# Performance work log

Measured on AMD Instinct MI355X. Metric: run time of the kernel, lower is better.

Reference implementation:

```python
import jax, jax.numpy as jnp
import numpy as np

D_MODEL = 512
N_HEADS = 8
D_HEAD = D_MODEL // N_HEADS
D_FF = 2048
LN_EPS = 1e-5


def _layer_norm(x, g, b):
    mu = jnp.mean(x, axis=-1, keepdims=True)
    var = jnp.var(x, axis=-1, keepdims=True)
    return (x - mu) * jax.lax.rsqrt(var + LN_EPS) * g + b


def setup_inputs() -> dict:
    key = jax.random.key(0)
    ks = jax.random.split(key, 16)
    s_d = 1.0 / np.sqrt(D_MODEL)
    s_f = 1.0 / np.sqrt(D_FF)
    x = jax.random.normal(ks[0], (32, 512, D_MODEL), dtype=jnp.float32)
    # per-head Q/K/V linears stacked over heads: [H, D, dh] weights, [H, dh] biases
    Wq = jax.random.uniform(ks[1], (N_HEADS, D_MODEL, D_HEAD), jnp.float32, -s_d, s_d)
    bq = jax.random.uniform(ks[2], (N_HEADS, D_HEAD), jnp.float32, -s_d, s_d)
    Wk = jax.random.uniform(ks[3], (N_HEADS, D_MODEL, D_HEAD), jnp.float32, -s_d, s_d)
    bk = jax.random.uniform(ks[4], (N_HEADS, D_HEAD), jnp.float32, -s_d, s_d)
    Wv = jax.random.uniform(ks[5], (N_HEADS, D_MODEL, D_HEAD), jnp.float32, -s_d, s_d)
    bv = jax.random.uniform(ks[6], (N_HEADS, D_HEAD), jnp.float32, -s_d, s_d)
    Wo = jax.random.uniform(ks[7], (D_MODEL, D_MODEL), jnp.float32, -s_d, s_d)
    bo = jax.random.uniform(ks[8], (D_MODEL,), jnp.float32, -s_d, s_d)
    ln1_g = jnp.ones((D_MODEL,), jnp.float32)
    ln1_b = jnp.zeros((D_MODEL,), jnp.float32)
    W1 = jax.random.uniform(ks[9], (D_MODEL, D_FF), jnp.float32, -s_d, s_d)
    b1 = jax.random.uniform(ks[10], (D_FF,), jnp.float32, -s_d, s_d)
    W2 = jax.random.uniform(ks[11], (D_FF, D_MODEL), jnp.float32, -s_f, s_f)
    b2 = jax.random.uniform(ks[12], (D_MODEL,), jnp.float32, -s_f, s_f)
    ln2_g = jnp.ones((D_MODEL,), jnp.float32)
    ln2_b = jnp.zeros((D_MODEL,), jnp.float32)
    return dict(x=x, Wq=Wq, bq=bq, Wk=Wk, bk=bk, Wv=Wv, bv=bv, Wo=Wo, bo=bo,
                ln1_g=ln1_g, ln1_b=ln1_b, W1=W1, b1=b1, W2=W2, b2=b2,
                ln2_g=ln2_g, ln2_b=ln2_b)


def reference(x, Wq, bq, Wk, bk, Wv, bv, Wo, bo, ln1_g, ln1_b, W1, b1, W2, b2, ln2_g, ln2_b):
    B, T, D = x.shape
    # batched-heads Q/K/V: [B, H, T, dh]
    q = jnp.einsum('btd,hde->bhte', x, Wq) + bq[None, :, None, :]
    k = jnp.einsum('btd,hde->bhte', x, Wk) + bk[None, :, None, :]
    v = jnp.einsum('btd,hde->bhte', x, Wv) + bv[None, :, None, :]
    scale = D_HEAD ** -0.5
    scores = jnp.einsum('bhte,bhse->bhts', q, k) * scale  # [B,H,T,T]
    causal = jnp.tril(jnp.ones((T, T), dtype=bool))
    scores = jnp.where(causal[None, None], scores, -jnp.inf)
    w = jax.nn.softmax(scores, axis=-1)
    o = jnp.einsum('bhts,bhse->bhte', w, v)              # [B,H,T,dh]
    o = jnp.transpose(o, (0, 2, 1, 3)).reshape(B, T, D)   # concat heads
    attn = o @ Wo + bo
    out1 = x + _layer_norm(attn, ln1_g, ln1_b)            # post-LN on sublayer output (as in source)
    ff = jax.nn.relu(out1 @ W1 + b1) @ W2 + b2
    return out1 + _layer_norm(ff, ln2_g, ln2_b)
```

## Files before the change

### kernel.cpp

```cpp
#include <hip/hip_runtime.h>
#include <hip/hip_bf16.h>


#define D_MODEL 512
#define N_HEADS 8
#define D_HEAD 64
#define D_FF 2048
#define NROWS 16384

typedef __bf16 bf16x8 __attribute__((ext_vector_type(8)));
typedef float f32x4 __attribute__((ext_vector_type(4)));

#define SWZ(x) ((x) ^ ((((x) >> 7) & 7) << 4))

static __device__ __forceinline__ ushort f2bf(float f) {
    union { float f; unsigned u; } v; v.f = f;
    unsigned r = v.u + 0x7fffu + ((v.u >> 16) & 1u);
    return (ushort)(r >> 16);
}
static __device__ __forceinline__ unsigned pack2(float lo, float hi) {
    return (unsigned)f2bf(lo) | ((unsigned)f2bf(hi) << 16);
}
static __device__ __forceinline__ void async16(const void* g, void* l) {
    __builtin_amdgcn_global_load_lds(
        (const __attribute__((address_space(1))) void*)g,
        (__attribute__((address_space(3))) void*)l, 16, 0, 0);
}

__global__ __launch_bounds__(256) void conv_bf_kernel(
    const float* __restrict__ src, ushort* __restrict__ dst, int n8)
{
    int i = blockIdx.x * 256 + threadIdx.x;
    if (i >= n8) return;
    const float4* s = (const float4*)src;
    float4 a = s[i * 2], b = s[i * 2 + 1];
    uint4 o;
    o.x = pack2(a.x, a.y); o.y = pack2(a.z, a.w);
    o.z = pack2(b.x, b.y); o.w = pack2(b.z, b.w);
    ((uint4*)dst)[i] = o;
}

static __device__ __forceinline__ void tile_transpose_body(
    const float* __restrict__ src, int srcldc, ushort* __restrict__ dst, int Rd,
    int r0, int c0)
{
    __shared__ float t[64][65];
    int tid = threadIdx.x;
    int lr = tid >> 4, lc4 = (tid & 15) * 4;
    #pragma unroll
    for (int i = 0; i < 4; ++i) {
        float4 v = *(const float4*)&src[(size_t)(r0 + lr + i * 16) * srcldc + c0 + lc4];
        t[lr + i * 16][lc4 + 0] = v.x;
        t[lr + i * 16][lc4 + 1] = v.y;
        t[lr + i * 16][lc4 + 2] = v.z;
        t[lr + i * 16][lc4 + 3] = v.w;
    }
    __syncthreads();
    int oc = tid >> 2, orr = (tid & 3) * 16;
    uint4 u0, u1;
    u0.x = pack2(t[orr + 0][oc],  t[orr + 1][oc]);
    u0.y = pack2(t[orr + 2][oc],  t[orr + 3][oc]);
    u0.z = pack2(t[orr + 4][oc],  t[orr + 5][oc]);
    u0.w = pack2(t[orr + 6][oc],  t[orr + 7][oc]);
    u1.x = pack2(t[orr + 8][oc],  t[orr + 9][oc]);
    u1.y = pack2(t[orr + 10][oc], t[orr + 11][oc]);
    u1.z = pack2(t[orr + 12][oc], t[orr + 13][oc]);
    u1.w = pack2(t[orr + 14][oc], t[orr + 15][oc]);
    ushort* d = dst + (size_t)(c0 + oc) * Rd + r0 + orr;
    *(uint4*)&d[0] = u0;
    *(uint4*)&d[8] = u1;
}

__global__ __launch_bounds__(256) void transpose_bf_kernel(
    const float* __restrict__ src, ushort* __restrict__ dst, int R, int C)
{
    tile_transpose_body(src, C, dst, R, blockIdx.y * 64, blockIdx.x * 64);
}

__global__ __launch_bounds__(256) void qkv_pack_kernel(
    const float* __restrict__ Wq, const float* __restrict__ Wk,
    const float* __restrict__ Wv, ushort* __restrict__ WpT)
{
    int z = blockIdx.z;
    int p = z >> 3, h = z & 7;
    const float* src = ((p == 0) ? Wq : (p == 1) ? Wk : Wv) + (size_t)h * D_MODEL * D_HEAD;
    ushort* dst = WpT + (size_t)(p * D_MODEL + h * D_HEAD) * D_MODEL;
    tile_transpose_body(src, D_HEAD, dst, D_MODEL, blockIdx.y * 64, 0);
}

__global__ __launch_bounds__(256) void pack_bias_kernel(
    const float* __restrict__ bq, const float* __restrict__ bk,
    const float* __restrict__ bv, float* __restrict__ bp)
{
    int idx = blockIdx.x * 256 + threadIdx.x;
    if (idx >= 3 * D_MODEL) return;
    int p = idx / D_MODEL;
    int h = (idx % D_MODEL) / D_HEAD;
    int e = idx % D_HEAD;
    const float* bb = (p == 0) ? bq : (p == 1) ? bk : bv;
    bp[idx] = bb[h * D_HEAD + e];
}

template<int OMODE, bool RELU>
__global__ __launch_bounds__(256) void gemm_bf16_kernel(
    const ushort* __restrict__ A, const ushort* __restrict__ BT,
    const float* __restrict__ bias, void* __restrict__ Cout,
    ushort* __restrict__ Qg, ushort* __restrict__ Kg, ushort* __restrict__ Vt,
    int M, int N, int K)
{
    __shared__ __align__(16) __bf16 As[128 * 64];
    __shared__ __align__(16) __bf16 Bs[128 * 64];

    const int tid = threadIdx.x;
    const int w = tid >> 6, l = tid & 63;
    const int wr = w >> 1, wc = w & 1;
    const int m0 = blockIdx.y * 128, n0 = blockIdx.x * 128;

    const ushort* Ag = A + (size_t)(m0 + w * 8 + l / 8) * K + (l % 8) * 8;
    const ushort* Bg = BT + (size_t)(n0 + w * 8 + l / 8) * K + (l % 8) * 8;
    __bf16* Asw = As + w * 512 + l * 8;
    __bf16* Bsw = Bs + w * 512 + l * 8;

    const int fr = l & 15, fq = l >> 4;
    const int a_base = (wr * 64 + fr) * 64 + fq * 8;
    const int b_base = (wc * 64 + fr) * 64 + fq * 8;

    f32x4 acc[4][4] = {};

    for (int k0 = 0; k0 < K; k0 += 64) {
        #pragma unroll
        for (int i = 0; i < 4; ++i) {
            async16(Ag + k0 + (size_t)i * 32 * K, Asw + i * 2048);
            async16(Bg + k0 + (size_t)i * 32 * K, Bsw + i * 2048);
        }
        __syncthreads();
        #pragma unroll
        for (int ks = 0; ks < 2; ++ks) {
            bf16x8 af[4], bfv[4];
            #pragma unroll
            for (int mi = 0; mi < 4; ++mi)
                af[mi] = *(const bf16x8*)&As[a_base + mi * 1024 + ks * 32];
            #pragma unroll
            for (int ni = 0; ni < 4; ++ni)
                bfv[ni] = *(const bf16x8*)&Bs[b_base + ni * 1024 + ks * 32];
            #pragma unroll
            for (int mi = 0; mi < 4; ++mi)
                #pragma unroll
                for (int ni = 0; ni < 4; ++ni)
                    acc[mi][ni] = __builtin_amdgcn_mfma_f32_16x16x32_bf16(
                        af[mi], bfv[ni], acc[mi][ni], 0, 0, 0);
        }
        __syncthreads();
    }

    #pragma unroll
    for (int ni = 0; ni < 4; ++ni) {
        int c = n0 + wc * 64 + ni * 16 + fr;
        float bv = bias ? bias[c] : 0.f;
        #pragma unroll
        for (int mi = 0; mi < 4; ++mi) {
            int r0 = m0 + wr * 64 + mi * 16 + fq * 4;
            float vv[4];
            #pragma unroll
            for (int reg = 0; reg < 4; ++reg) {
                float v = acc[mi][ni][reg] + bv;
                if (RELU) v = fmaxf(v, 0.f);
                vv[reg] = v;
            }
            if (OMODE == 0) {
                #pragma unroll
                for (int reg = 0; reg < 4; ++reg)
                    ((float*)Cout)[(size_t)(r0 + reg) * N + c] = vv[reg];
            } else if (OMODE == 1) {
                #pragma unroll
                for (int reg = 0; reg < 4; ++reg)
                    ((ushort*)Cout)[(size_t)(r0 + reg) * N + c] = f2bf(vv[reg]);
            } else {
                int p = n0 >> 9;
                int h = (c >> 6) & 7, e = c & 63;
                int b = r0 >> 9, t0 = r0 & 511;
                size_t bh = (size_t)(b * 8 + h);
                if (p == 2) {
                    uint2 pk;
                    pk.x = pack2(vv[0], vv[1]);
                    pk.y = pack2(vv[2], vv[3]);
                    *(uint2*)&Vt[bh * 32768 + (size_t)e * 512 + t0] = pk;
                } else {
                    ushort* dst = (p == 0 ? Qg : Kg) + bh * 32768 + (size_t)t0 * 64 + e;
                    #pragma unroll
                    for (int reg = 0; reg < 4; ++reg)
                        dst[reg * 64] = f2bf(vv[reg]);
                }
            }
        }
    }
}

__global__ __launch_bounds__(256) void attn_kernel(
    const ushort* __restrict__ Qg,
    const ushort* __restrict__ Kg,
    const ushort* __restrict__ Vt,
    ushort* __restrict__ O)
{
    __shared__ __align__(16) char QP[8192];
    __shared__ __align__(16) char KB[2][8192];
    __shared__ __align__(16) char VB[2][8192];

    const int bh = blockIdx.x, qb = blockIdx.y;
    const int tid = threadIdx.x;
    const int w = tid >> 6, l = tid & 63;

    const ushort* Qb = Qg + (size_t)bh * 32768;
    const ushort* Kb = Kg + (size_t)bh * 32768;
    const ushort* Vb = Vt + (size_t)bh * 32768;

    #pragma unroll
    for (int i = 0; i < 2; ++i) {
        int Xi = i * 4096 + tid * 16;
        int row = Xi >> 7;
        int sw = SWZ(Xi) & 127;
        async16((const char*)(Qb + (size_t)(qb * 64 + row) * 64) + sw, QP + Xi);
    }
    #define STAGEKV(kt, bb)                                                     \
        { _Pragma("unroll")                                                     \
          for (int i = 0; i < 2; ++i) {                                         \
              int Xi = i * 4096 + tid * 16;                                     \
              int row = Xi >> 7;                                                \
              int sw = SWZ(Xi) & 127;                                           \
              async16((const char*)(Kb + (size_t)((kt) * 64 + row) * 64) + sw,  \
                      KB[bb] + Xi);                                             \
              async16((const char*)(Vb + (size_t)row * 512 + (kt) * 64) + sw,   \
                      VB[bb] + Xi);                                             \
          } }
    STAGEKV(0, 0);
    __syncthreads();

    bf16x8 qf[2];
    {
        int qrow = w * 16 + (l & 15);
        #pragma unroll
        for (int ks = 0; ks < 2; ++ks) {
            int X = qrow * 128 + ks * 64 + (l >> 4) * 16;
            qf[ks] = *(const bf16x8*)(QP + SWZ(X));
        }
    }

    float mrow = -INFINITY, lrow = 0.f;
    f32x4 oacc[4] = {};
// ... 37 lines not shown
        float psum = 0.f;
        #pragma unroll
        for (int i = 0; i < 16; ++i) { sv[i] = __expf(sv[i] - mnew); psum += sv[i]; }
        psum += __shfl_xor(psum, 16);
        psum += __shfl_xor(psum, 32);
        lrow = lrow * corr + psum;

        #pragma unroll
        for (int mi = 0; mi < 4; ++mi) {
            uint2 pk;
            pk.x = pack2(sv[mi * 4 + 0], sv[mi * 4 + 1]);
            pk.y = pack2(sv[mi * 4 + 2], sv[mi * 4 + 3]);
            int X = qrow_t * 128 + (mi * 16 + (l >> 4) * 4) * 2;
            *(uint2*)(QP + SWZ(X)) = pk;
        }

        #pragma unroll
        for (int r = 0; r < 4; ++r) {
            float cr = __shfl(corr, (l & 48) | ((l >> 4) * 4 + r));
            #pragma unroll
            for (int n = 0; n < 4; ++n) oacc[n][r] *= cr;
        }

        #pragma unroll
        for (int ks = 0; ks < 2; ++ks) {
            int Xa = qrow_t * 128 + ks * 64 + (l >> 4) * 16;
            bf16x8 pa = *(const bf16x8*)(QP + SWZ(Xa));
            #pragma unroll
            for (int n = 0; n < 4; ++n) {
                int Xb = (n * 16 + (l & 15)) * 128 + ks * 64 + (l >> 4) * 16;
                bf16x8 vb = *(const bf16x8*)(VB[cur] + SWZ(Xb));
                oacc[n] = __builtin_amdgcn_mfma_f32_16x16x32_bf16(
                    pa, vb, oacc[n], 0, 0, 0);
            }
        }
        __syncthreads();
    }

    float linv = 1.0f / lrow;
    const int b_ = bh >> 3, h_ = bh & 7;
    #pragma unroll
    for (int r = 0; r < 4; ++r) {
        float li = __shfl(linv, (l & 48) | ((l >> 4) * 4 + r));
        int trow = qb * 64 + w * 16 + (l >> 4) * 4 + r;
        size_t obase = ((size_t)b_ * 512 + trow) * 512 + h_ * 64 + (l & 15);
        #pragma unroll
        for (int n = 0; n < 4; ++n)
            O[obase + n * 16] = f2bf(oacc[n][r] * li);
    }
}

template<bool WBF>
__global__ __launch_bounds__(256) void ln_res_kernel(
    const float* __restrict__ v, const float* __restrict__ res,
    const float* __restrict__ g, const float* __restrict__ bb,
    float* __restrict__ out, ushort* __restrict__ out_bf)
{
    int row  = blockIdx.x * 4 + (threadIdx.x >> 6);
    int lane = threadIdx.x & 63;
    const float4* vp = (const float4*)(v + (size_t)row * D_MODEL);
    float4 a = vp[lane];
    float4 c = vp[lane + 64];
    float sum = a.x + a.y + a.z + a.w + c.x + c.y + c.z + c.w;
    float sq  = a.x*a.x + a.y*a.y + a.z*a.z + a.w*a.w
              + c.x*c.x + c.y*c.y + c.z*c.z + c.w*c.w;
    #pragma unroll
    for (int o = 1; o < 64; o <<= 1) {
        sum += __shfl_xor(sum, o);
        sq  += __shfl_xor(sq, o);
    }
    float mu   = sum * (1.f / 512.f);
    float var  = sq * (1.f / 512.f) - mu * mu;
    float rstd = rsqrtf(var + 1e-5f);

    const float4* rp = (const float4*)(res + (size_t)row * D_MODEL);
    const float4* gp = (const float4*)g;
    const float4* bp = (const float4*)bb;
    float4 r0 = rp[lane], r1 = rp[lane + 64];
    float4 g0 = gp[lane], g1 = gp[lane + 64];
    float4 b0 = bp[lane], b1 = bp[lane + 64];
    float4 o0, o1;
    o0.x = r0.x + (a.x - mu) * rstd * g0.x + b0.x;
    o0.y = r0.y + (a.y - mu) * rstd * g0.y + b0.y;
    o0.z = r0.z + (a.z - mu) * rstd * g0.z + b0.z;
    o0.w = r0.w + (a.w - mu) * rstd * g0.w + b0.w;
    o1.x = r1.x + (c.x - mu) * rstd * g1.x + b1.x;
    o1.y = r1.y + (c.y - mu) * rstd * g1.y + b1.y;
    o1.z = r1.z + (c.z - mu) * rstd * g1.z + b1.z;
    o1.w = r1.w + (c.w - mu) * rstd * g1.w + b1.w;
    float4* op = (float4*)(out + (size_t)row * D_MODEL);
    op[lane] = o0;
    op[lane + 64] = o1;
    if (WBF) {
        uint2 p0, p1;
        p0.x = pack2(o0.x, o0.y); p0.y = pack2(o0.z, o0.w);
        p1.x = pack2(o1.x, o1.y); p1.y = pack2(o1.z, o1.w);
        *(uint2*)&out_bf[(size_t)row * D_MODEL + lane * 4] = p0;
        *(uint2*)&out_bf[(size_t)row * D_MODEL + 256 + lane * 4] = p1;
    }
}

extern "C" void kernel_launch(void* const* d_in, const int* in_sizes, int n_in,
                              void* d_out, int out_size, void* d_ws, size_t ws_size,
                              hipStream_t stream)
{
    const float* x     = (const float*)d_in[0];
    const float* Wq    = (const float*)d_in[1];
    const float* bq    = (const float*)d_in[2];
    const float* Wk    = (const float*)d_in[3];
    const float* bk    = (const float*)d_in[4];
    const float* Wv    = (const float*)d_in[5];
    const float* bv    = (const float*)d_in[6];
    const float* Wo    = (const float*)d_in[7];
    const float* bo    = (const float*)d_in[8];
    const float* ln1_g = (const float*)d_in[9];
    const float* ln1_b = (const float*)d_in[10];
    const float* W1    = (const float*)d_in[11];
    const float* b1    = (const float*)d_in[12];
    const float* W2    = (const float*)d_in[13];
    const float* b2    = (const float*)d_in[14];
    const float* ln2_g = (const float*)d_in[15];
    const float* ln2_b = (const float*)d_in[16];

    float* ws = (float*)d_ws;
    ushort* Qg      = (ushort*)(ws);
    ushort* Kg      = (ushort*)(ws + 4194304);
    ushort* Vt      = (ushort*)(ws + 8388608);
    ushort* O_bf    = (ushort*)(ws + 12582912);
    float*  attnb   = ws + 16777216;
    float*  out1    = ws + 25165824;
    ushort* out1_bf = (ushort*)(ws + 33554432);
    ushort* x_bf    = (ushort*)(ws + 37748736);
    ushort* WpT     = (ushort*)(ws + 41943040);
    ushort* WoT     = (ushort*)(ws + 42336256);
    ushort* W1T     = (ushort*)(ws + 42467328);
    ushort* W2T     = (ushort*)(ws + 42991616);
    float*  bp      = ws + 43515904;
    ushort* ff1_bf  = (ushort*)ws;
    float*  ff2     = attnb;

    conv_bf_kernel<<<dim3(4096), 256, 0, stream>>>(x, x_bf, NROWS * D_MODEL / 8);
    qkv_pack_kernel<<<dim3(1, 8, 24), 256, 0, stream>>>(Wq, Wk, Wv, WpT);
    transpose_bf_kernel<<<dim3(8, 8), 256, 0, stream>>>(Wo, WoT, 512, 512);
    transpose_bf_kernel<<<dim3(32, 8), 256, 0, stream>>>(W1, W1T, 512, 2048);
    transpose_bf_kernel<<<dim3(8, 32), 256, 0, stream>>>(W2, W2T, 2048, 512);
    pack_bias_kernel<<<dim3(6), 256, 0, stream>>>(bq, bk, bv, bp);

    gemm_bf16_kernel<2, false><<<dim3(12, 128), 256, 0, stream>>>(
        x_bf, WpT, bp, nullptr, Qg, Kg, Vt, NROWS, 1536, 512);

    attn_kernel<<<dim3(256, 8), 256, 0, stream>>>(Qg, Kg, Vt, O_bf);

    gemm_bf16_kernel<0, false><<<dim3(4, 128), 256, 0, stream>>>(
        O_bf, WoT, bo, attnb, nullptr, nullptr, nullptr, NROWS, 512, 512);

    ln_res_kernel<true><<<dim3(NROWS / 4), 256, 0, stream>>>(
        attnb, x, ln1_g, ln1_b, out1, out1_bf);

    gemm_bf16_kernel<1, true><<<dim3(16, 128), 256, 0, stream>>>(
        out1_bf, W1T, b1, ff1_bf, nullptr, nullptr, nullptr, NROWS, 2048, 512);

    gemm_bf16_kernel<0, false><<<dim3(4, 128), 256, 0, stream>>>(
        ff1_bf, W2T, b2, ff2, nullptr, nullptr, nullptr, NROWS, 512, 2048);

    ln_res_kernel<false><<<dim3(NROWS / 4), 256, 0, stream>>>(
        ff2, out1, ln2_g, ln2_b, (float*)d_out, nullptr);
}
```

Measured before the change: 264.0 us.

## Rewrite bf16 GEMM with double-buffered LDS, 32x32 MFMA, swizzle, larger tiles

The GEMM kernel now uses 256x128 tiles with 512 threads, 32x32x16 MFMA instructions, XOR-swizzled LDS layout, and a double-buffered async global-to-LDS pipeline that uses a single barrier per k-step. A flat grid with an XCD-aware block remap replaces the 2D grid. The aim is to overlap loads with MFMA compute, reduce LDS bank conflicts, and improve data reuse per block. In exchange it needs 96KB of dynamic shared memory per block, allowing only one block per CU, and the epilogue store pattern changes.

```diff
diff --git a/kernel.cpp b/kernel.cpp
--- a/kernel.cpp
+++ b/kernel.cpp
@@ -10,6 +10,7 @@
 
 typedef __bf16 bf16x8 __attribute__((ext_vector_type(8)));
 typedef float f32x4 __attribute__((ext_vector_type(4)));
+typedef float f32x16 __attribute__((ext_vector_type(16)));
 
 #define SWZ(x) ((x) ^ ((((x) >> 7) & 7) << 4))
 
@@ -102,98 +103,137 @@
 }
 
 template<int OMODE, bool RELU>
-__global__ __launch_bounds__(256) void gemm_bf16_kernel(
+__global__ __launch_bounds__(512, 1) void gemm_bf16_kernel(
     const ushort* __restrict__ A, const ushort* __restrict__ BT,
     const float* __restrict__ bias, void* __restrict__ Cout,
     ushort* __restrict__ Qg, ushort* __restrict__ Kg, ushort* __restrict__ Vt,
-    int M, int N, int K)
-{
-    __shared__ __align__(16) __bf16 As[128 * 64];
-    __shared__ __align__(16) __bf16 Bs[128 * 64];
+    int M, int N, int K, int nbx)
+{
+    extern __shared__ __align__(16) char smem[];
 
     const int tid = threadIdx.x;
-    const int w = tid >> 6, l = tid & 63;
-    const int wr = w >> 1, wc = w & 1;
-    const int m0 = blockIdx.y * 128, n0 = blockIdx.x * 128;
-
-    const ushort* Ag = A + (size_t)(m0 + w * 8 + l / 8) * K + (l % 8) * 8;
-    const ushort* Bg = BT + (size_t)(n0 + w * 8 + l / 8) * K + (l % 8) * 8;
-    __bf16* Asw = As + w * 512 + l * 8;
-    __bf16* Bsw = Bs + w * 512 + l * 8;
-
-    const int fr = l & 15, fq = l >> 4;
-    const int a_base = (wr * 64 + fr) * 64 + fq * 8;
-    const int b_base = (wc * 64 + fr) * 64 + fq * 8;
-
-    f32x4 acc[4][4] = {};
-
-    for (int k0 = 0; k0 < K; k0 += 64) {
-        #pragma unroll
-        for (int i = 0; i < 4; ++i) {
-            async16(Ag + k0 + (size_t)i * 32 * K, Asw + i * 2048);
-            async16(Bg + k0 + (size_t)i * 32 * K, Bsw + i * 2048);
-        }
-        __syncthreads();
-        #pragma unroll
-        for (int ks = 0; ks < 2; ++ks) {
-            bf16x8 af[4], bfv[4];
-            #pragma unroll
-            for (int mi = 0; mi < 4; ++mi)
-                af[mi] = *(const bf16x8*)&As[a_base + mi * 1024 + ks * 32];
-            #pragma unroll
-            for (int ni = 0; ni < 4; ++ni)
-                bfv[ni] = *(const bf16x8*)&Bs[b_base + ni * 1024 + ks * 32];
-            #pragma unroll
-            for (int mi = 0; mi < 4; ++mi)
+    const int wid = tid >> 6, l = tid & 63;
+    const int wr = wid >> 1, wc = wid & 1;
+
+    const int total = gridDim.x;
+    const int cpx = total >> 3;
+    const int flat = blockIdx.x;
+    const int swz = (flat & 7) * cpx + (flat >> 3);
+    const int bx = swz % nbx, by = swz / nbx;
+    const int m0 = by * 256, n0 = bx * 128;
+
+    const int srow = tid >> 3;
+    const int sbyte = (tid & 7) * 16;
+    const int ssw = sbyte ^ ((srow & 7) << 4);
+
+    #define STAGE(t)                                                          \
+    {                                                                         \
+        const int kk_ = (t) * 64;                                             \
+        char* dst_ = smem + ((t) & 1) * 49152;                                \
+        _Pragma("unroll")                                                     \
+        for (int i = 0; i < 4; ++i)                                           \
+            async16((const char*)(A + (size_t)(m0 + i * 64 + srow) * K + kk_) \
+                        + ssw,                                                \
+                    dst_ + i * 8192 + tid * 16);                              \
+        _Pragma("unroll")                                                     \
+        for (int i = 0; i < 2; ++i)                                           \
+            async16((const char*)(BT + (size_t)(n0 + i * 64 + srow) * K + kk_)\
+                        + ssw,                                                \
+                    dst_ + 32768 + i * 8192 + tid * 16);                      \
+    }
+
+    const int fl = l & 31, fh = l >> 5;
+    const int frsw = (fl & 7) << 4;
+
+    f32x16 acc[2][2] = {};
+
+    STAGE(0);
+    const int T = K >> 6;
+    for (int t = 0; t < T; ++t) {
+        __builtin_amdgcn_s_barrier();
+        if (t + 1 < T) {
+            STAGE(t + 1);
+            asm volatile("s_waitcnt vmcnt(6)" ::: "memory");
+        } else {
+            asm volatile("s_waitcnt vmcnt(0)" ::: "memory");
+        }
+        __builtin_amdgcn_sched_barrier(0);
+
+        const char* bufA = smem + (t & 1) * 49152;
+        const char* bufB = bufA + 32768;
+        #pragma unroll
+        for (int ks = 0; ks < 4; ++ks) {
+            const int kb = ((ks * 32 + fh * 16) ^ frsw);
+            bf16x8 af[2], bfv[2];
+            #pragma unroll
+            for (int mi = 0; mi < 2; ++mi)
+                af[mi] = *(const bf16x8*)(bufA +
+                    (wr * 64 + mi * 32 + fl) * 128 + kb);
+            #pragma unroll
+            for (int ni = 0; ni < 2; ++ni)
+                bfv[ni] = *(const bf16x8*)(bufB +
+                    (wc * 64 + ni * 32 + fl) * 128 + kb);
+            #pragma unroll
+            for (int mi = 0; mi < 2; ++mi)
                 #pragma unroll
-                for (int ni = 0; ni < 4; ++ni)
-                    acc[mi][ni] = __builtin_amdgcn_mfma_f32_16x16x32_bf16(
+                for (int ni = 0; ni < 2; ++ni)
+                    acc[mi][ni] = __builtin_amdgcn_mfma_f32_32x32x16_bf16(
                         af[mi], bfv[ni], acc[mi][ni], 0, 0, 0);
         }
-        __syncthreads();
     }
 
     #pragma unroll
-    for (int ni = 0; ni < 4; ++ni) {
-        int c = n0 + wc * 64 + ni * 16 + fr;
-        float bv = bias ? bias[c] : 0.f;
-        #pragma unroll
-        for (int mi = 0; mi < 4; ++mi) {
-            int r0 = m0 + wr * 64 + mi * 16 + fq * 4;
-            float vv[4];
-            #pragma unroll
-            for (int reg = 0; reg < 4; ++reg) {
-                float v = acc[mi][ni][reg] + bv;
+    for (int ni = 0; ni < 2; ++ni) {
+        const int c = n0 + wc * 64 + ni * 32 + fl;
+        const float bvv = bias ? bias[c] : 0.f;
+        #pragma unroll
+        for (int mi = 0; mi < 2; ++mi) {
+            const int rbase = m0 + wr * 64 + mi * 32 + (fh << 2);
+            float vv[16];
+            #pragma unroll
+            for (int reg = 0; reg < 16; ++reg) {
+                float v = acc[mi][ni][reg] + bvv;
                 if (RELU) v = fmaxf(v, 0.f);
                 vv[reg] = v;
             }
             if (OMODE == 0) {
                 #pragma unroll
-                for (int reg = 0; reg < 4; ++reg)
-                    ((float*)Cout)[(size_t)(r0 + reg) * N + c] = vv[reg];
+                for (int reg = 0; reg < 16; ++reg) {
+                    int r = rbase + (reg & 3) + ((reg >> 2) << 3);
+                    ((float*)Cout)[(size_t)r * N + c] = vv[reg];
+                }
             } else if (OMODE == 1) {
                 #pragma unroll
-                for (int reg = 0; reg < 4; ++reg)
-                    ((ushort*)Cout)[(size_t)(r0 + reg) * N + c] = f2bf(vv[reg]);
+                for (int reg = 0; reg < 16; ++reg) {
+                    int r = rbase + (reg & 3) + ((reg >> 2) << 3);
+                    ((ushort*)Cout)[(size_t)r * N + c] = f2bf(vv[reg]);
+                }
             } else {
-                int p = n0 >> 9;
-                int h = (c >> 6) & 7, e = c & 63;
-                int b = r0 >> 9, t0 = r0 & 511;
-                size_t bh = (size_t)(b * 8 + h);
-                if (p == 2) {
-                    uint2 pk;
-                    pk.x = pack2(vv[0], vv[1]);
-                    pk.y = pack2(vv[2], vv[3]);
-                    *(uint2*)&Vt[bh * 32768 + (size_t)e * 512 + t0] = pk;
-                } else {
-                    ushort* dst = (p == 0 ? Qg : Kg) + bh * 32768 + (size_t)t0 * 64 + e;
-                    #pragma unroll
-                    for (int reg = 0; reg < 4; ++reg)
-                        dst[reg * 64] = f2bf(vv[reg]);
+                const int p = n0 >> 9;
+                const int h = (c >> 6) & 7, e = c & 63;
+                #pragma unroll
+                for (int q = 0; q < 4; ++q) {
+                    int r0 = rbase + (q << 3);
+                    int b = r0 >> 9, t0 = r0 & 511;
+                    size_t bh = (size_t)(b * 8 + h);
+                    if (p == 2) {
+                        uint2 pk;
+                        pk.x = pack2(vv[q * 4 + 0], vv[q * 4 + 1]);
+                        pk.y = pack2(vv[q * 4 + 2], vv[q * 4 + 3]);
+                        *(uint2*)&Vt[bh * 32768 + (size_t)e * 512 + t0] = pk;
+                    } else {
+                        ushort* dst = (p == 0 ? Qg : Kg) + bh * 32768 +
+                                      (size_t)t0 * 64 + e;
+                        dst[0]   = f2bf(vv[q * 4 + 0]);
+                        dst[64]  = f2bf(vv[q * 4 + 1]);
+                        dst[128] = f2bf(vv[q * 4 + 2]);
+                        dst[192] = f2bf(vv[q * 4 + 3]);
+                    }
                 }
             }
         }
     }
+    #undef STAGE
 }
 
 __global__ __launch_bounds__(256) void attn_kernel(
@@ -424,6 +464,16 @@
     ushort* ff1_bf  = (ushort*)ws;
     float*  ff2     = attnb;
 
+    (void)hipFuncSetAttribute(
+        reinterpret_cast<const void*>(&gemm_bf16_kernel<2, false>),
+        hipFuncAttributeMaxDynamicSharedMemorySize, 98304);
+    (void)hipFuncSetAttribute(
+        reinterpret_cast<const void*>(&gemm_bf16_kernel<0, false>),
+        hipFuncAttributeMaxDynamicSharedMemorySize, 98304);
+    (void)hipFuncSetAttribute(
+        reinterpret_cast<const void*>(&gemm_bf16_kernel<1, true>),
+        hipFuncAttributeMaxDynamicSharedMemorySize, 98304);
+
     conv_bf_kernel<<<dim3(4096), 256, 0, stream>>>(x, x_bf, NROWS * D_MODEL / 8);
     qkv_pack_kernel<<<dim3(1, 8, 24), 256, 0, stream>>>(Wq, Wk, Wv, WpT);
     transpose_bf_kernel<<<dim3(8, 8), 256, 0, stream>>>(Wo, WoT, 512, 512);
@@ -431,22 +481,22 @@
     transpose_bf_kernel<<<dim3(8, 32), 256, 0, stream>>>(W2, W2T, 2048, 512);
     pack_bias_kernel<<<dim3(6), 256, 0, stream>>>(bq, bk, bv, bp);
 
-    gemm_bf16_kernel<2, false><<<dim3(12, 128), 256, 0, stream>>>(
-        x_bf, WpT, bp, nullptr, Qg, Kg, Vt, NROWS, 1536, 512);
+    gemm_bf16_kernel<2, false><<<dim3(768), 512, 98304, stream>>>(
+        x_bf, WpT, bp, nullptr, Qg, Kg, Vt, NROWS, 1536, 512, 12);
 
     attn_kernel<<<dim3(256, 8), 256, 0, stream>>>(Qg, Kg, Vt, O_bf);
 
-    gemm_bf16_kernel<0, false><<<dim3(4, 128), 256, 0, stream>>>(
-        O_bf, WoT, bo, attnb, nullptr, nullptr, nullptr, NROWS, 512, 512);
+    gemm_bf16_kernel<0, false><<<dim3(256), 512, 98304, stream>>>(
+        O_bf, WoT, bo, attnb, nullptr, nullptr, nullptr, NROWS, 512, 512, 4);
 
     ln_res_kernel<true><<<dim3(NROWS / 4), 256, 0, stream>>>(
         attnb, x, ln1_g, ln1_b, out1, out1_bf);
 
-    gemm_bf16_kernel<1, true><<<dim3(16, 128), 256, 0, stream>>>(
-        out1_bf, W1T, b1, ff1_bf, nullptr, nullptr, nullptr, NROWS, 2048, 512);
-
-    gemm_bf16_kernel<0, false><<<dim3(4, 128), 256, 0, stream>>>(
-        ff1_bf, W2T, b2, ff2, nullptr, nullptr, nullptr, NROWS, 512, 2048);
+    gemm_bf16_kernel<1, true><<<dim3(1024), 512, 98304, stream>>>(
+        out1_bf, W1T, b1, ff1_bf, nullptr, nullptr, nullptr, NROWS, 2048, 512, 16);
+
+    gemm_bf16_kernel<0, false><<<dim3(256), 512, 98304, stream>>>(
+        ff1_bf, W2T, b2, ff2, nullptr, nullptr, nullptr, NROWS, 512, 2048, 4);
 
     ln_res_kernel<false><<<dim3(NROWS / 4), 256, 0, stream>>>(
         ff2, out1, ln2_g, ln2_b, (float*)d_out, nullptr);
```

Result: faster. 224.0 us (-15.1%).

## Replace GEMM with double-buffered 256-row tile kernel using swizzled LDS and prefetch

Applied to the files above, without the earlier changes.

Replaces the 128x128 single-buffer bf16 GEMM with a 512-thread kernel computing 256xNF*64 tiles. It double-buffers A/B in dynamic LDS with XOR-swizzled rows and issues the next K-tile's async loads mid-iteration, using vmcnt waits and raw barriers so loads overlap MFMA work. It also adds an XCD-aware block index swizzle and s_setprio around the MFMA bursts. The goal is to cut global-load stalls and raise data reuse per block. The cost is up to 128KB of LDS and one block per CU, which lowers occupancy and depends on fragile hand-tuned waitcnt counts.

```diff
diff --git a/kernel.cpp b/kernel.cpp
--- a/kernel.cpp
+++ b/kernel.cpp
@@ -101,69 +101,145 @@
     bp[idx] = bb[h * D_HEAD + e];
 }
 
-template<int OMODE, bool RELU>
-__global__ __launch_bounds__(256) void gemm_bf16_kernel(
+template<int NF, int OMODE, bool RELU>
+__global__ __launch_bounds__(512, 1) void gemm8p_kernel(
     const ushort* __restrict__ A, const ushort* __restrict__ BT,
     const float* __restrict__ bias, void* __restrict__ Cout,
     ushort* __restrict__ Qg, ushort* __restrict__ Kg, ushort* __restrict__ Vt,
-    int M, int N, int K)
-{
-    __shared__ __align__(16) __bf16 As[128 * 64];
-    __shared__ __align__(16) __bf16 Bs[128 * 64];
+    int M, int N, int K, int nbx)
+{
+    extern __shared__ __align__(16) char smem[];
+    constexpr int ABYTES = 32768;
+    constexpr int PAR = ABYTES + NF * 8192;
 
     const int tid = threadIdx.x;
-    const int w = tid >> 6, l = tid & 63;
-    const int wr = w >> 1, wc = w & 1;
-    const int m0 = blockIdx.y * 128, n0 = blockIdx.x * 128;
-
-    const ushort* Ag = A + (size_t)(m0 + w * 8 + l / 8) * K + (l % 8) * 8;
-    const ushort* Bg = BT + (size_t)(n0 + w * 8 + l / 8) * K + (l % 8) * 8;
-    __bf16* Asw = As + w * 512 + l * 8;
-    __bf16* Bsw = Bs + w * 512 + l * 8;
+    const int wid = tid >> 6, l = tid & 63;
+    const int wm = wid >> 2, wn = wid & 3;
+
+    const int cpx = gridDim.x >> 3;
+    const int flat = blockIdx.x;
+    const int swz = (flat & 7) * cpx + (flat >> 3);
+    const int bx = swz % nbx, by = swz / nbx;
+    const int m0 = by * 256, n0 = bx * (NF * 64);
+
+    const char* Ac = (const char*)A;
+    const char* Bc = (const char*)BT;
+    const size_t K2 = (size_t)K * 2;
+    const int T = K >> 6;
+
+    const int srow = tid >> 3;
+    const int ssw  = ((tid & 7) ^ (srow & 7)) << 4;
+
+    #define STG_A(t, q_) async16(Ac + (size_t)(m0 + (q_) * 64 + srow) * K2 +  \
+                                     (size_t)(t) * 128 + ssw,                 \
+                                 smem + (((t) & 1) ? PAR : 0) + (q_) * 8192 + \
+                                     tid * 16)
+    #define STG_B(t, q_) async16(Bc + (size_t)(n0 + (q_) * 64 + srow) * K2 +  \
+                                     (size_t)(t) * 128 + ssw,                 \
+                                 smem + (((t) & 1) ? PAR : 0) + ABYTES +      \
+                                     (q_) * 8192 + tid * 16)
+    #define P0SET(t) do { if constexpr (NF == 4) {                            \
+                              STG_B(t,0); STG_B(t,1); STG_B(t,2); STG_B(t,3);}\
+                          else { STG_A(t,0); STG_A(t,2);                      \
+                                 STG_B(t,0); STG_B(t,1); } } while (0)
+    #define P1SET(t) do { if constexpr (NF == 4) {                            \
+                              STG_A(t,0); STG_A(t,2); STG_A(t,1); STG_A(t,3);}\
+                          else { STG_A(t,1); STG_A(t,3); } } while (0)
 
     const int fr = l & 15, fq = l >> 4;
-    const int a_base = (wr * 64 + fr) * 64 + fq * 8;
-    const int b_base = (wc * 64 + fr) * 64 + fq * 8;
-
-    f32x4 acc[4][4] = {};
-
-    for (int k0 = 0; k0 < K; k0 += 64) {
-        #pragma unroll
-        for (int i = 0; i < 4; ++i) {
-            async16(Ag + k0 + (size_t)i * 32 * K, Asw + i * 2048);
-            async16(Bg + k0 + (size_t)i * 32 * K, Bsw + i * 2048);
-        }
-        __syncthreads();
-        #pragma unroll
-        for (int ks = 0; ks < 2; ++ks) {
-            bf16x8 af[4], bfv[4];
+    const int rsw = (fr & 7) << 4;
+
+    f32x4 acc[8][NF] = {};
+
+    P0SET(0);
+    P1SET(0);
+    asm volatile("s_waitcnt vmcnt(2)" ::: "memory");
+    __builtin_amdgcn_s_barrier();
+    __builtin_amdgcn_sched_barrier(0);
+
+    for (int t = 0; t < T; ++t) {
+        const char* par = smem + ((t & 1) ? PAR : 0);
+        #pragma unroll
+        for (int S = 0; S < 2; ++S) {
+            const char* bufA = par + (wm * 2 + S) * 8192;
+            bf16x8 af[4][2];
             #pragma unroll
             for (int mi = 0; mi < 4; ++mi)
-                af[mi] = *(const bf16x8*)&As[a_base + mi * 1024 + ks * 32];
-            #pragma unroll
-            for (int ni = 0; ni < 4; ++ni)
-                bfv[ni] = *(const bf16x8*)&Bs[b_base + ni * 1024 + ks * 32];
+                #pragma unroll
+                for (int ks = 0; ks < 2; ++ks)
+                    af[mi][ks] = *(const bf16x8*)(bufA + (mi * 16 + fr) * 128 +
+                        ((ks * 64 + fq * 16) ^ rsw));
+            bf16x8 bf0[NF / 2][2], bf1[NF / 2][2];
+            #pragma unroll
+            for (int nj = 0; nj < NF / 2; ++nj)
+                #pragma unroll
+                for (int ks = 0; ks < 2; ++ks) {
+                    int grow = wn * (NF * 16) + nj * 16 + fr;
+                    bf0[nj][ks] = *(const bf16x8*)(par + ABYTES +
+                        (grow >> 6) * 8192 + (grow & 63) * 128 +
+                        ((ks * 64 + fq * 16) ^ rsw));
+                }
+            if (t + 1 < T) { if (S == 0) P0SET(t + 1); else P1SET(t + 1); }
+            #pragma unroll
+            for (int nj = 0; nj < NF / 2; ++nj)
+                #pragma unroll
+                for (int ks = 0; ks < 2; ++ks) {
+                    int grow = wn * (NF * 16) + (NF / 2) * 16 + nj * 16 + fr;
+                    bf1[nj][ks] = *(const bf16x8*)(par + ABYTES +
+                        (grow >> 6) * 8192 + (grow & 63) * 128 +
+                        ((ks * 64 + fq * 16) ^ rsw));
+                }
+
+            __builtin_amdgcn_s_setprio(1);
             #pragma unroll
             for (int mi = 0; mi < 4; ++mi)
                 #pragma unroll
-                for (int ni = 0; ni < 4; ++ni)
-                    acc[mi][ni] = __builtin_amdgcn_mfma_f32_16x16x32_bf16(
-                        af[mi], bfv[ni], acc[mi][ni], 0, 0, 0);
-        }
-        __syncthreads();
-    }
+                for (int nj = 0; nj < NF / 2; ++nj) {
+                    f32x4 a = acc[S * 4 + mi][nj];
+                    a = __builtin_amdgcn_mfma_f32_16x16x32_bf16(af[mi][0], bf0[nj][0], a, 0, 0, 0);
+                    a = __builtin_amdgcn_mfma_f32_16x16x32_bf16(af[mi][1], bf0[nj][1], a, 0, 0, 0);
+                    acc[S * 4 + mi][nj] = a;
+                }
+            __builtin_amdgcn_s_setprio(0);
+            __builtin_amdgcn_s_setprio(1);
+            #pragma unroll
+            for (int mi = 0; mi < 4; ++mi)
+                #pragma unroll
+                for (int nj = 0; nj < NF / 2; ++nj) {
+                    f32x4 a = acc[S * 4 + mi][NF / 2 + nj];
+                    a = __builtin_amdgcn_mfma_f32_16x16x32_bf16(af[mi][0], bf1[nj][0], a, 0, 0, 0);
+                    a = __builtin_amdgcn_mfma_f32_16x16x32_bf16(af[mi][1], bf1[nj][1], a, 0, 0, 0);
+                    acc[S * 4 + mi][NF / 2 + nj] = a;
+                }
+            __builtin_amdgcn_s_setprio(0);
+
+            if (S == 0) {
+                if (t + 1 < T) asm volatile("s_waitcnt vmcnt(4)" ::: "memory");
+                else           asm volatile("s_waitcnt vmcnt(0)" ::: "memory");
+            } else {
+                if (t + 1 < T) asm volatile("s_waitcnt vmcnt(2)" ::: "memory");
+                else           asm volatile("s_waitcnt vmcnt(0)" ::: "memory");
+            }
+            __builtin_amdgcn_s_barrier();
+            __builtin_amdgcn_sched_barrier(0);
+        }
+    }
+    #undef STG_A
+    #undef STG_B
+    #undef P0SET
+    #undef P1SET
 
     #pragma unroll
-    for (int ni = 0; ni < 4; ++ni) {
-        int c = n0 + wc * 64 + ni * 16 + fr;
-        float bv = bias ? bias[c] : 0.f;
-        #pragma unroll
-        for (int mi = 0; mi < 4; ++mi) {
-            int r0 = m0 + wr * 64 + mi * 16 + fq * 4;
+    for (int mi = 0; mi < 8; ++mi) {
+        const int r0 = m0 + wm * 128 + mi * 16 + fq * 4;
+        #pragma unroll
+        for (int nf = 0; nf < NF; ++nf) {
+            const int c = n0 + wn * (NF * 16) + nf * 16 + fr;
+            const float bvv = bias ? bias[c] : 0.f;
             float vv[4];
             #pragma unroll
             for (int reg = 0; reg < 4; ++reg) {
-                float v = acc[mi][ni][reg] + bv;
+                float v = acc[mi][nf][reg] + bvv;
                 if (RELU) v = fmaxf(v, 0.f);
                 vv[reg] = v;
             }
@@ -176,20 +252,22 @@
                 for (int reg = 0; reg < 4; ++reg)
                     ((ushort*)Cout)[(size_t)(r0 + reg) * N + c] = f2bf(vv[reg]);
             } else {
-                int p = n0 >> 9;
-                int h = (c >> 6) & 7, e = c & 63;
-                int b = r0 >> 9, t0 = r0 & 511;
-                size_t bh = (size_t)(b * 8 + h);
+                const int p = n0 >> 9;
+                const int h = (c >> 6) & 7, e = c & 63;
+                const int b = r0 >> 9, t0 = r0 & 511;
+                const size_t bh = (size_t)(b * 8 + h);
                 if (p == 2) {
                     uint2 pk;
                     pk.x = pack2(vv[0], vv[1]);
                     pk.y = pack2(vv[2], vv[3]);
                     *(uint2*)&Vt[bh * 32768 + (size_t)e * 512 + t0] = pk;
                 } else {
-                    ushort* dst = (p == 0 ? Qg : Kg) + bh * 32768 + (size_t)t0 * 64 + e;
-                    #pragma unroll
-                    for (int reg = 0; reg < 4; ++reg)
-                        dst[reg * 64] = f2bf(vv[reg]);
+                    ushort* dst = (p == 0 ? Qg : Kg) + bh * 32768 +
+                                  (size_t)t0 * 64 + e;
+                    dst[0]   = f2bf(vv[0]);
+                    dst[64]  = f2bf(vv[1]);
+                    dst[128] = f2bf(vv[2]);
+                    dst[192] = f2bf(vv[3]);
                 }
             }
         }
@@ -424,6 +502,16 @@
     ushort* ff1_bf  = (ushort*)ws;
     float*  ff2     = attnb;
 
+    (void)hipFuncSetAttribute(
+        reinterpret_cast<const void*>(&gemm8p_kernel<4, 2, false>),
+        hipFuncAttributeMaxDynamicSharedMemorySize, 131072);
+    (void)hipFuncSetAttribute(
+        reinterpret_cast<const void*>(&gemm8p_kernel<4, 1, true>),
+        hipFuncAttributeMaxDynamicSharedMemorySize, 131072);
+    (void)hipFuncSetAttribute(
+        reinterpret_cast<const void*>(&gemm8p_kernel<2, 0, false>),
+        hipFuncAttributeMaxDynamicSharedMemorySize, 98304);
+
     conv_bf_kernel<<<dim3(4096), 256, 0, stream>>>(x, x_bf, NROWS * D_MODEL / 8);
     qkv_pack_kernel<<<dim3(1, 8, 24), 256, 0, stream>>>(Wq, Wk, Wv, WpT);
     transpose_bf_kernel<<<dim3(8, 8), 256, 0, stream>>>(Wo, WoT, 512, 512);
@@ -431,22 +519,22 @@
     transpose_bf_kernel<<<dim3(8, 32), 256, 0, stream>>>(W2, W2T, 2048, 512);
     pack_bias_kernel<<<dim3(6), 256, 0, stream>>>(bq, bk, bv, bp);
 
-    gemm_bf16_kernel<2, false><<<dim3(12, 128), 256, 0, stream>>>(
-        x_bf, WpT, bp, nullptr, Qg, Kg, Vt, NROWS, 1536, 512);
+    gemm8p_kernel<4, 2, false><<<dim3(384), 512, 131072, stream>>>(
+        x_bf, WpT, bp, nullptr, Qg, Kg, Vt, NROWS, 1536, 512, 6);
 
     attn_kernel<<<dim3(256, 8), 256, 0, stream>>>(Qg, Kg, Vt, O_bf);
 
-    gemm_bf16_kernel<0, false><<<dim3(4, 128), 256, 0, stream>>>(
-        O_bf, WoT, bo, attnb, nullptr, nullptr, nullptr, NROWS, 512, 512);
+    gemm8p_kernel<2, 0, false><<<dim3(256), 512, 98304, stream>>>(
+        O_bf, WoT, bo, attnb, nullptr, nullptr, nullptr, NROWS, 512, 512, 4);
 
     ln_res_kernel<true><<<dim3(NROWS / 4), 256, 0, stream>>>(
         attnb, x, ln1_g, ln1_b, out1, out1_bf);
 
-    gemm_bf16_kernel<1, true><<<dim3(16, 128), 256, 0, stream>>>(
-        out1_bf, W1T, b1, ff1_bf, nullptr, nullptr, nullptr, NROWS, 2048, 512);
-
-    gemm_bf16_kernel<0, false><<<dim3(4, 128), 256, 0, stream>>>(
-        ff1_bf, W2T, b2, ff2, nullptr, nullptr, nullptr, NROWS, 512, 2048);
+    gemm8p_kernel<4, 1, true><<<dim3(512), 512, 131072, stream>>>(
+        out1_bf, W1T, b1, ff1_bf, nullptr, nullptr, nullptr, NROWS, 2048, 512, 8);
+
+    gemm8p_kernel<2, 0, false><<<dim3(256), 512, 98304, stream>>>(
+        ff1_bf, W2T, b2, ff2, nullptr, nullptr, nullptr, NROWS, 512, 2048, 4);
 
     ln_res_kernel<false><<<dim3(NROWS / 4), 256, 0, stream>>>(
         ff2, out1, ln2_g, ln2_b, (float*)d_out, nullptr);
```

Result: faster. 234.9 us (-11.0%).

## Replace GEMMs with 512-thread double-buffered kernel and bf16 pre-LN outputs

Applied to the files above, without the earlier changes.

Replaces the 128x128 GEMM with a templated 512-thread kernel. It stages only A tiles in LDS with XOR swizzle and double buffering, reads B fragments directly from global memory into registers, and remaps blocks with a swizzle for L2 locality. It also sets MFMA priority around the compute loop and uses larger 256x256 tiles for the QKV and FF1 GEMMs. The Wo and W2 GEMM outputs are now stored as bf16 instead of fp32, and the LayerNorm kernels read bf16. This halves that intermediate traffic at the cost of rounding the pre-LN activations.

```diff
diff --git a/kernel.cpp b/kernel.cpp
--- a/kernel.cpp
+++ b/kernel.cpp
@@ -20,6 +20,10 @@
 }
 static __device__ __forceinline__ unsigned pack2(float lo, float hi) {
     return (unsigned)f2bf(lo) | ((unsigned)f2bf(hi) << 16);
+}
+static __device__ __forceinline__ float bf2f(ushort u) {
+    union { unsigned u; float f; } v; v.u = (unsigned)u << 16;
+    return v.f;
 }
 static __device__ __forceinline__ void async16(const void* g, void* l) {
     __builtin_amdgcn_global_load_lds(
@@ -101,69 +105,109 @@
     bp[idx] = bb[h * D_HEAD + e];
 }
 
-template<int OMODE, bool RELU>
-__global__ __launch_bounds__(256) void gemm_bf16_kernel(
+template<int QM, int NF, int OMODE, bool RELU>
+__global__ __launch_bounds__(512, 1) void gemmv3_kernel(
     const ushort* __restrict__ A, const ushort* __restrict__ BT,
     const float* __restrict__ bias, void* __restrict__ Cout,
     ushort* __restrict__ Qg, ushort* __restrict__ Kg, ushort* __restrict__ Vt,
-    int M, int N, int K)
-{
-    __shared__ __align__(16) __bf16 As[128 * 64];
-    __shared__ __align__(16) __bf16 Bs[128 * 64];
+    int N, int K, int nbx)
+{
+    extern __shared__ __align__(16) char smem[];
 
     const int tid = threadIdx.x;
-    const int w = tid >> 6, l = tid & 63;
-    const int wr = w >> 1, wc = w & 1;
-    const int m0 = blockIdx.y * 128, n0 = blockIdx.x * 128;
-
-    const ushort* Ag = A + (size_t)(m0 + w * 8 + l / 8) * K + (l % 8) * 8;
-    const ushort* Bg = BT + (size_t)(n0 + w * 8 + l / 8) * K + (l % 8) * 8;
-    __bf16* Asw = As + w * 512 + l * 8;
-    __bf16* Bsw = Bs + w * 512 + l * 8;
+    const int wid = tid >> 6, l = tid & 63;
+    const int wm = wid >> 2, wn = wid & 3;
+
+    const int cpx = gridDim.x >> 3;
+    const int flat = blockIdx.x;
+    const int swz = (flat & 7) * cpx + (flat >> 3);
+    const int bx = swz % nbx, by = swz / nbx;
+    const int m0 = by * (QM * 64), n0 = bx * (NF * 64);
+
+    const char* Ac = (const char*)A;
+    const char* Bc = (const char*)BT;
+    const size_t K2 = (size_t)K * 2;
+    const int T = K >> 6;
+
+    const int srow = tid >> 3;
+    const int ssw  = ((tid & 7) ^ (srow & 7)) << 4;
 
     const int fr = l & 15, fq = l >> 4;
-    const int a_base = (wr * 64 + fr) * 64 + fq * 8;
-    const int b_base = (wc * 64 + fr) * 64 + fq * 8;
-
-    f32x4 acc[4][4] = {};
-
-    for (int k0 = 0; k0 < K; k0 += 64) {
-        #pragma unroll
-        for (int i = 0; i < 4; ++i) {
-            async16(Ag + k0 + (size_t)i * 32 * K, Asw + i * 2048);
-            async16(Bg + k0 + (size_t)i * 32 * K, Bsw + i * 2048);
+    const int rsw = (fr & 7) << 4;
+
+    const char* browp[NF];
+    #pragma unroll
+    for (int nf = 0; nf < NF; ++nf)
+        browp[nf] = Bc + (size_t)(n0 + wn * (NF * 16) + nf * 16 + fr) * K2 + fq * 16;
+
+    f32x4 acc[QM * 2][NF] = {};
+
+    #pragma unroll
+    for (int q = 0; q < QM; ++q)
+        async16(Ac + (size_t)(m0 + q * 64 + srow) * K2 + ssw,
+                smem + q * 8192 + tid * 16);
+    __syncthreads();
+
+    for (int t = 0; t < T; ++t) {
+        const char* par = smem + ((t & 1) ? QM * 8192 : 0);
+
+        bf16x8 bfr[NF][2];
+        #pragma unroll
+        for (int nf = 0; nf < NF; ++nf)
+            #pragma unroll
+            for (int ks = 0; ks < 2; ++ks)
+                bfr[nf][ks] = *(const bf16x8*)(browp[nf] +
+                    (size_t)t * 128 + ks * 64);
+
+        if (t + 1 < T) {
+            #pragma unroll
+            for (int q = 0; q < QM; ++q)
+                async16(Ac + (size_t)(m0 + q * 64 + srow) * K2 +
+                            (size_t)(t + 1) * 128 + ssw,
+                        smem + (((t + 1) & 1) ? QM * 8192 : 0) + q * 8192 +
+                            tid * 16);
+        }
+
+        #pragma unroll
+        for (int S = 0; S < 2; ++S) {
+            bf16x8 af[QM][2];
+            #pragma unroll
+            for (int mi = 0; mi < QM; ++mi) {
+                const int absrow = wm * (QM * 32) + (S * QM + mi) * 16;
+                const int q = absrow >> 6, rin = absrow & 63;
+                #pragma unroll
+                for (int ks = 0; ks < 2; ++ks)
+                    af[mi][ks] = *(const bf16x8*)(par + q * 8192 +
+                        (rin + fr) * 128 + ((ks * 64 + fq * 16) ^ rsw));
+            }
+            __builtin_amdgcn_s_setprio(1);
+            #pragma unroll
+            for (int mi = 0; mi < QM; ++mi)
+                #pragma unroll
+                for (int nf = 0; nf < NF; ++nf) {
+                    f32x4 a = acc[S * QM + mi][nf];
+                    a = __builtin_amdgcn_mfma_f32_16x16x32_bf16(
+                        af[mi][0], bfr[nf][0], a, 0, 0, 0);
+                    a = __builtin_amdgcn_mfma_f32_16x16x32_bf16(
+                        af[mi][1], bfr[nf][1], a, 0, 0, 0);
+                    acc[S * QM + mi][nf] = a;
+                }
+            __builtin_amdgcn_s_setprio(0);
         }
         __syncthreads();
-        #pragma unroll
-        for (int ks = 0; ks < 2; ++ks) {
-            bf16x8 af[4], bfv[4];
-            #pragma unroll
-            for (int mi = 0; mi < 4; ++mi)
-                af[mi] = *(const bf16x8*)&As[a_base + mi * 1024 + ks * 32];
-            #pragma unroll
-            for (int ni = 0; ni < 4; ++ni)
-                bfv[ni] = *(const bf16x8*)&Bs[b_base + ni * 1024 + ks * 32];
-            #pragma unroll
-            for (int mi = 0; mi < 4; ++mi)
-                #pragma unroll
-                for (int ni = 0; ni < 4; ++ni)
-                    acc[mi][ni] = __builtin_amdgcn_mfma_f32_16x16x32_bf16(
-                        af[mi], bfv[ni], acc[mi][ni], 0, 0, 0);
-        }
-        __syncthreads();
-    }
-
-    #pragma unroll
-    for (int ni = 0; ni < 4; ++ni) {
-        int c = n0 + wc * 64 + ni * 16 + fr;
-        float bv = bias ? bias[c] : 0.f;
-        #pragma unroll
-        for (int mi = 0; mi < 4; ++mi) {
-            int r0 = m0 + wr * 64 + mi * 16 + fq * 4;
+    }
+
+    #pragma unroll
+    for (int miA = 0; miA < QM * 2; ++miA) {
+        const int r0 = m0 + wm * (QM * 32) + miA * 16 + fq * 4;
+        #pragma unroll
+        for (int nf = 0; nf < NF; ++nf) {
+            const int c = n0 + wn * (NF * 16) + nf * 16 + fr;
+            const float bvv = bias ? bias[c] : 0.f;
             float vv[4];
             #pragma unroll
             for (int reg = 0; reg < 4; ++reg) {
-                float v = acc[mi][ni][reg] + bv;
+                float v = acc[miA][nf][reg] + bvv;
                 if (RELU) v = fmaxf(v, 0.f);
                 vv[reg] = v;
             }
@@ -176,20 +220,22 @@
                 for (int reg = 0; reg < 4; ++reg)
                     ((ushort*)Cout)[(size_t)(r0 + reg) * N + c] = f2bf(vv[reg]);
             } else {
-                int p = n0 >> 9;
-                int h = (c >> 6) & 7, e = c & 63;
-                int b = r0 >> 9, t0 = r0 & 511;
-                size_t bh = (size_t)(b * 8 + h);
+                const int p = n0 >> 9;
+                const int h = (c >> 6) & 7, e = c & 63;
+                const int b = r0 >> 9, t0 = r0 & 511;
+                const size_t bh = (size_t)(b * 8 + h);
                 if (p == 2) {
                     uint2 pk;
                     pk.x = pack2(vv[0], vv[1]);
                     pk.y = pack2(vv[2], vv[3]);
                     *(uint2*)&Vt[bh * 32768 + (size_t)e * 512 + t0] = pk;
                 } else {
-                    ushort* dst = (p == 0 ? Qg : Kg) + bh * 32768 + (size_t)t0 * 64 + e;
-                    #pragma unroll
-                    for (int reg = 0; reg < 4; ++reg)
-                        dst[reg * 64] = f2bf(vv[reg]);
+                    ushort* dst = (p == 0 ? Qg : Kg) + bh * 32768 +
+                                  (size_t)t0 * 64 + e;
+                    dst[0]   = f2bf(vv[0]);
+                    dst[64]  = f2bf(vv[1]);
+                    dst[128] = f2bf(vv[2]);
+                    dst[192] = f2bf(vv[3]);
                 }
             }
         }
@@ -337,18 +383,24 @@
 
 template<bool WBF>
 __global__ __launch_bounds__(256) void ln_res_kernel(
-    const float* __restrict__ v, const float* __restrict__ res,
+    const ushort* __restrict__ v, const float* __restrict__ res,
     const float* __restrict__ g, const float* __restrict__ bb,
     float* __restrict__ out, ushort* __restrict__ out_bf)
 {
     int row  = blockIdx.x * 4 + (threadIdx.x >> 6);
     int lane = threadIdx.x & 63;
-    const float4* vp = (const float4*)(v + (size_t)row * D_MODEL);
-    float4 a = vp[lane];
-    float4 c = vp[lane + 64];
-    float sum = a.x + a.y + a.z + a.w + c.x + c.y + c.z + c.w;
-    float sq  = a.x*a.x + a.y*a.y + a.z*a.z + a.w*a.w
-              + c.x*c.x + c.y*c.y + c.z*c.z + c.w*c.w;
+    const int c0 = lane * 8;
+
+    uint4 vb = *(const uint4*)&v[(size_t)row * D_MODEL + c0];
+    float f[8];
+    f[0] = bf2f((ushort)(vb.x & 0xffff)); f[1] = bf2f((ushort)(vb.x >> 16));
+    f[2] = bf2f((ushort)(vb.y & 0xffff)); f[3] = bf2f((ushort)(vb.y >> 16));
+    f[4] = bf2f((ushort)(vb.z & 0xffff)); f[5] = bf2f((ushort)(vb.z >> 16));
+    f[6] = bf2f((ushort)(vb.w & 0xffff)); f[7] = bf2f((ushort)(vb.w >> 16));
+
+    float sum = 0.f, sq = 0.f;
+    #pragma unroll
+    for (int i = 0; i < 8; ++i) { sum += f[i]; sq += f[i] * f[i]; }
     #pragma unroll
     for (int o = 1; o < 64; o <<= 1) {
         sum += __shfl_xor(sum, o);
@@ -358,30 +410,29 @@
     float var  = sq * (1.f / 512.f) - mu * mu;
     float rstd = rsqrtf(var + 1e-5f);
 
-    const float4* rp = (const float4*)(res + (size_t)row * D_MODEL);
-    const float4* gp = (const float4*)g;
-    const float4* bp = (const float4*)bb;
-    float4 r0 = rp[lane], r1 = rp[lane + 64];
-    float4 g0 = gp[lane], g1 = gp[lane + 64];
-    float4 b0 = bp[lane], b1 = bp[lane + 64];
-    float4 o0, o1;
-    o0.x = r0.x + (a.x - mu) * rstd * g0.x + b0.x;
-    o0.y = r0.y + (a.y - mu) * rstd * g0.y + b0.y;
-    o0.z = r0.z + (a.z - mu) * rstd * g0.z + b0.z;
-    o0.w = r0.w + (a.w - mu) * rstd * g0.w + b0.w;
-    o1.x = r1.x + (c.x - mu) * rstd * g1.x + b1.x;
-    o1.y = r1.y + (c.y - mu) * rstd * g1.y + b1.y;
-    o1.z = r1.z + (c.z - mu) * rstd * g1.z + b1.z;
-    o1.w = r1.w + (c.w - mu) * rstd * g1.w + b1.w;
-    float4* op = (float4*)(out + (size_t)row * D_MODEL);
-    op[lane] = o0;
-    op[lane + 64] = o1;
+    float4 r0 = *(const float4*)&res[(size_t)row * D_MODEL + c0];
+    float4 r1 = *(const float4*)&res[(size_t)row * D_MODEL + c0 + 4];
+    float4 g0 = *(const float4*)&g[c0],  g1 = *(const float4*)&g[c0 + 4];
+    float4 b0 = *(const float4*)&bb[c0], b1 = *(const float4*)&bb[c0 + 4];
+
+    float o8[8];
+    o8[0] = r0.x + (f[0] - mu) * rstd * g0.x + b0.x;
+    o8[1] = r0.y + (f[1] - mu) * rstd * g0.y + b0.y;
+    o8[2] = r0.z + (f[2] - mu) * rstd * g0.z + b0.z;
+    o8[3] = r0.w + (f[3] - mu) * rstd * g0.w + b0.w;
+    o8[4] = r1.x + (f[4] - mu) * rstd * g1.x + b1.x;
+    o8[5] = r1.y + (f[5] - mu) * rstd * g1.y + b1.y;
+    o8[6] = r1.z + (f[6] - mu) * rstd * g1.z + b1.z;
+    o8[7] = r1.w + (f[7] - mu) * rstd * g1.w + b1.w;
+
+    float4* op = (float4*)&out[(size_t)row * D_MODEL + c0];
+    op[0] = make_float4(o8[0], o8[1], o8[2], o8[3]);
+    op[1] = make_float4(o8[4], o8[5], o8[6], o8[7]);
     if (WBF) {
-        uint2 p0, p1;
-        p0.x = pack2(o0.x, o0.y); p0.y = pack2(o0.z, o0.w);
-        p1.x = pack2(o1.x, o1.y); p1.y = pack2(o1.z, o1.w);
-        *(uint2*)&out_bf[(size_t)row * D_MODEL + lane * 4] = p0;
-        *(uint2*)&out_bf[(size_t)row * D_MODEL + 256 + lane * 4] = p1;
+        uint4 pk;
+        pk.x = pack2(o8[0], o8[1]); pk.y = pack2(o8[2], o8[3]);
+        pk.z = pack2(o8[4], o8[5]); pk.w = pack2(o8[6], o8[7]);
+        *(uint4*)&out_bf[(size_t)row * D_MODEL + c0] = pk;
     }
 }
 
@@ -412,17 +463,27 @@
     ushort* Kg      = (ushort*)(ws + 4194304);
     ushort* Vt      = (ushort*)(ws + 8388608);
     ushort* O_bf    = (ushort*)(ws + 12582912);
-    float*  attnb   = ws + 16777216;
-    float*  out1    = ws + 25165824;
-    ushort* out1_bf = (ushort*)(ws + 33554432);
-    ushort* x_bf    = (ushort*)(ws + 37748736);
+    ushort* attn_bf = (ushort*)(ws + 16777216);
+    float*  out1    = ws + 20971520;
+    ushort* out1_bf = (ushort*)(ws + 29360128);
+    ushort* x_bf    = (ushort*)(ws + 33554432);
+    ushort* ff2_bf  = (ushort*)(ws + 37748736);
     ushort* WpT     = (ushort*)(ws + 41943040);
     ushort* WoT     = (ushort*)(ws + 42336256);
     ushort* W1T     = (ushort*)(ws + 42467328);
     ushort* W2T     = (ushort*)(ws + 42991616);
     float*  bp      = ws + 43515904;
     ushort* ff1_bf  = (ushort*)ws;
-    float*  ff2     = attnb;
+
+    (void)hipFuncSetAttribute(
+        reinterpret_cast<const void*>(&gemmv3_kernel<4, 4, 2, false>),
+        hipFuncAttributeMaxDynamicSharedMemorySize, 65536);
+    (void)hipFuncSetAttribute(
+        reinterpret_cast<const void*>(&gemmv3_kernel<4, 4, 1, true>),
+        hipFuncAttributeMaxDynamicSharedMemorySize, 65536);
+    (void)hipFuncSetAttribute(
+        reinterpret_cast<const void*>(&gemmv3_kernel<2, 2, 1, false>),
+        hipFuncAttributeMaxDynamicSharedMemorySize, 32768);
 
     conv_bf_kernel<<<dim3(4096), 256, 0, stream>>>(x, x_bf, NROWS * D_MODEL / 8);
     qkv_pack_kernel<<<dim3(1, 8, 24), 256, 0, stream>>>(Wq, Wk, Wv, WpT);
@@ -431,23 +492,23 @@
     transpose_bf_kernel<<<dim3(8, 32), 256, 0, stream>>>(W2, W2T, 2048, 512);
     pack_bias_kernel<<<dim3(6), 256, 0, stream>>>(bq, bk, bv, bp);
 
-    gemm_bf16_kernel<2, false><<<dim3(12, 128), 256, 0, stream>>>(
-        x_bf, WpT, bp, nullptr, Qg, Kg, Vt, NROWS, 1536, 512);
+    gemmv3_kernel<4, 4, 2, false><<<dim3(384), 512, 65536, stream>>>(
+        x_bf, WpT, bp, nullptr, Qg, Kg, Vt, 1536, 512, 6);
 
     attn_kernel<<<dim3(256, 8), 256, 0, stream>>>(Qg, Kg, Vt, O_bf);
 
-    gemm_bf16_kernel<0, false><<<dim3(4, 128), 256, 0, stream>>>(
-        O_bf, WoT, bo, attnb, nullptr, nullptr, nullptr, NROWS, 512, 512);
+    gemmv3_kernel<2, 2, 1, false><<<dim3(512), 512, 32768, stream>>>(
+        O_bf, WoT, bo, attn_bf, nullptr, nullptr, nullptr, 512, 512, 4);
 
     ln_res_kernel<true><<<dim3(NROWS / 4), 256, 0, stream>>>(
-        attnb, x, ln1_g, ln1_b, out1, out1_bf);
-
-    gemm_bf16_kernel<1, true><<<dim3(16, 128), 256, 0, stream>>>(
-        out1_bf, W1T, b1, ff1_bf, nullptr, nullptr, nullptr, NROWS, 2048, 512);
-
-    gemm_bf16_kernel<0, false><<<dim3(4, 128), 256, 0, stream>>>(
-        ff1_bf, W2T, b2, ff2, nullptr, nullptr, nullptr, NROWS, 512, 2048);
+        attn_bf, x, ln1_g, ln1_b, out1, out1_bf);
+
+    gemmv3_kernel<4, 4, 1, true><<<dim3(512), 512, 65536, stream>>>(
+        out1_bf, W1T, b1, ff1_bf, nullptr, nullptr, nullptr, 2048, 512, 8);
+
+    gemmv3_kernel<2, 2, 1, false><<<dim3(512), 512, 32768, stream>>>(
+        ff1_bf, W2T, b2, ff2_bf, nullptr, nullptr, nullptr, 512, 2048, 4);
 
     ln_res_kernel<false><<<dim3(NROWS / 4), 256, 0, stream>>>(
-        ff2, out1, ln2_g, ln2_b, (float*)d_out, nullptr);
-}
+        ff2_bf, out1, ln2_g, ln2_b, (float*)d_out, nullptr);
+}
```

Result: slower. 306.1 us (+16.0%).
